# Optimization experiments

Measured on AMD Instinct MI355X. Metric: run time of the kernel, lower is better.

## Reference

```python
import jax, jax.numpy as jnp
import numpy as np

B, H, E = 1024, 2048, 1024

def _xavier(key, shape):
    # torch xavier_normal_ on [1, out, in]: std = sqrt(2/(fan_in+fan_out)) over last two dims
    fan_out, fan_in = shape[-2], shape[-1]
    std = (2.0 / (fan_in + fan_out)) ** 0.5
    return jax.random.normal(key, shape, jnp.float32) * std

def setup_inputs() -> dict:
    key = jax.random.key(0)
    ks = jax.random.split(key, 17)
    inp = {
        'x': jax.random.normal(ks[0], (B, E, 1), jnp.float32),
        'c': jax.random.normal(ks[1], (B, H, 1), jnp.float32),
        'h': jax.random.normal(ks[2], (B, H, 1), jnp.float32),
        'W_xi': _xavier(ks[3], (1, H, E)), 'W_hi': _xavier(ks[4], (1, H, H)), 'B_i': _xavier(ks[5], (1, H, 1)),
        'W_xg': _xavier(ks[6], (1, H, E)), 'W_hg': _xavier(ks[7], (1, H, H)), 'B_g': _xavier(ks[8], (1, H, 1)),
        'W_xf': _xavier(ks[9], (1, H, E)), 'W_hf': _xavier(ks[10], (1, H, H)), 'B_f': _xavier(ks[11], (1, H, 1)),
        'W_xo': _xavier(ks[12], (1, H, E)), 'W_ho': _xavier(ks[13], (1, H, H)), 'B_o': _xavier(ks[14], (1, H, 1)),
        'W_hy': _xavier(ks[15], (1, E, H)), 'B_y': _xavier(ks[16], (1, E, 1)),
    }
    return inp

def reference(x, c, h, W_xi, W_hi, B_i, W_xg, W_hg, B_g, W_xf, W_hf, B_f, W_xo, W_ho, B_o, W_hy, B_y):
    # jnp.matmul broadcasts the leading batch dim: [1,H,E] @ [B,E,1] -> [B,H,1]
    i = jax.nn.sigmoid(jnp.matmul(W_xi, x) + jnp.matmul(W_hi, h) + B_i)
    g = jnp.tanh(jnp.matmul(W_xg, x) + jnp.matmul(W_hg, h) + B_g)
    f = jax.nn.sigmoid(jnp.matmul(W_xf, x) + jnp.matmul(W_hf, h) + B_f)
    c_new = f * c + i * g
    o = jax.nn.sigmoid(jnp.matmul(W_xo, x) + jnp.matmul(W_ho, h) + B_o)
    h_new = o * c_new  # NOTE: source uses o*c (no tanh), faithful to original
    y = jnp.tanh(jnp.matmul(W_hy, h_new) + B_y)
    return (y, c_new, h_new)
```

## Files before the change

### kernel.cpp

```cpp
#include <hip/hip_runtime.h>

#define B_SZ 1024
#define H_SZ 2048
#define E_SZ 1024

typedef float  f32x4 __attribute__((ext_vector_type(4)));
typedef short  s16x8 __attribute__((ext_vector_type(8)));

__device__ __forceinline__ unsigned short f2bf(float f) {
    unsigned u = __float_as_uint(f);
    u = u + 0x7fffu + ((u >> 16) & 1u);
    return (unsigned short)(u >> 16);
}
__device__ __forceinline__ float bf2f(unsigned short s) {
    return __uint_as_float(((unsigned)s) << 16);
}
__device__ __forceinline__ float sigm(float v) {
    return 1.0f / (1.0f + __expf(-v));
}
__device__ __forceinline__ unsigned cvtpk(float lo, float hi) {
    unsigned r;
    asm("v_cvt_pk_bf16_f32 %0, %1, %2" : "=v"(r) : "v"(lo), "v"(hi));
    return r;
}

__device__ __forceinline__ void gll(const unsigned short* g, unsigned short* l) {
    __builtin_amdgcn_global_load_lds(
        (const __attribute__((address_space(1))) unsigned int*)g,
        (__attribute__((address_space(3))) unsigned int*)l, 16, 0, 0);
}

struct CastArgs {
    const float*    src[2];
    unsigned short* dst[2];
    int             n[2];
};

__global__ __launch_bounds__(256) void cast_kernel(CastArgs a) {
    const int arr = blockIdx.y;
    const int n = a.n[arr];
    const float* __restrict__ s = a.src[arr];
    unsigned short* __restrict__ d = a.dst[arr];
    const int stride = gridDim.x * 256 * 4;
    for (int i = (blockIdx.x * 256 + threadIdx.x) * 4; i < n; i += stride) {
        float4 v = *(const float4*)(s + i);
        ushort4 o;
        o.x = f2bf(v.x); o.y = f2bf(v.y); o.z = f2bf(v.z); o.w = f2bf(v.w);
        *(ushort4*)(d + i) = o;
    }
}

__device__ __forceinline__ void gemm_bk128(
    const unsigned short* __restrict__ A,
    const float* __restrict__ W,
    int ld, int kLen, int m0, int n0,
    unsigned short* lA, unsigned short* lB,
    f32x4 acc[4][4], int t)
{
    const int lane = t & 63;
    const int w    = t >> 6;
    const int wr   = (w >> 1) << 6;
    const int wc   = (w & 1) << 6;
    const int lr   = lane & 15;
    const int q4   = lane >> 4;

    const int srow = t >> 4;
    const int sblk = ((t & 15) ^ srow) << 3;
    const unsigned short* gA = A + (size_t)(m0 + srow) * ld + sblk;
    const float*          gW = W + (size_t)(n0 + srow) * ld + sblk;
    const size_t st16 = (size_t)16 * ld;

    f32x4 f0[8], f1[8];
#pragma unroll
    for (int p = 0; p < 8; ++p) {
        const float* s = gW + p * st16;
        f0[p] = *(const f32x4*)(s);
        f1[p] = *(const f32x4*)(s + 4);
    }

    for (int k0 = 0; k0 < kLen; k0 += 128) {
#pragma unroll
        for (int p = 0; p < 8; ++p) {
            uint4 pk;
            pk.x = cvtpk(f0[p].x, f0[p].y);
            pk.y = cvtpk(f0[p].z, f0[p].w);
            pk.z = cvtpk(f1[p].x, f1[p].y);
            pk.w = cvtpk(f1[p].z, f1[p].w);
            *(uint4*)(lB + (t + 256 * p) * 8) = pk;
        }
#pragma unroll
        for (int p = 0; p < 8; ++p)
            gll(gA + k0 + p * st16, lA + (t + 256 * p) * 8);
        __syncthreads();

        if (k0 + 128 < kLen) {
#pragma unroll
            for (int p = 0; p < 8; ++p) {
                const float* s = gW + (k0 + 128) + p * st16;
                f0[p] = *(const f32x4*)(s);
                f1[p] = *(const f32x4*)(s + 4);
            }
        }

#pragma unroll
        for (int ks = 0; ks < 4; ++ks) {
            s16x8 af[4], bfr[4];
#pragma unroll
            for (int i = 0; i < 4; ++i) {
                const int ra = wr + i * 16 + lr;
                af[i] = *(const s16x8*)(lA + ra * 128 +
                         ((((ks << 2) + q4) ^ (ra & 15)) << 3));
            }
#pragma unroll
            for (int j = 0; j < 4; ++j) {
                const int rb = wc + j * 16 + lr;
                bfr[j] = *(const s16x8*)(lB + rb * 128 +
                          ((((ks << 2) + q4) ^ (rb & 15)) << 3));
            }
#pragma unroll
            for (int i = 0; i < 4; ++i)
#pragma unroll
                for (int j = 0; j < 4; ++j)
                    acc[i][j] = __builtin_amdgcn_mfma_f32_16x16x32_bf16(
                        af[i], bfr[j], acc[i][j], 0, 0, 0);
        }
        __syncthreads();
    }
}

struct GatesArgs {
    const unsigned short *Xb, *Hb;
    const float *Wx[4], *Wh[4], *bias[4];
    unsigned short *Z;
};

__global__ __launch_bounds__(256, 2) void gates_kernel(GatesArgs a) {
    __shared__ unsigned short lA[128 * 128];
    __shared__ unsigned short lB[128 * 128];
    const int t   = threadIdx.x;
    const int b   = blockIdx.x;
    const int xcd = b & 7;
    const int i_  = b >> 3;
    const int nt  = xcd * 8 + (i_ >> 3);
    const int m0  = (i_ & 7) * 128;
    const int q   = nt >> 4;
    const int n0  = (nt & 15) * 128;

    f32x4 acc[4][4] = {};
    gemm_bk128(a.Xb, a.Wx[q], E_SZ, E_SZ, m0, n0, lA, lB, acc, t);
    gemm_bk128(a.Hb, a.Wh[q], H_SZ, H_SZ, m0, n0, lA, lB, acc, t);

    const float* bias = a.bias[q];
    const int lane = t & 63, w = t >> 6;
    const int wr = (w >> 1) << 6, wc = (w & 1) << 6;
    const int lr = lane & 15, rq = (lane >> 4) << 2;
    unsigned short* Zq = a.Z + (size_t)q * B_SZ * H_SZ;
#pragma unroll
    for (int i = 0; i < 4; ++i) {
#pragma unroll
        for (int j = 0; j < 4; ++j) {
            const int n = n0 + wc + j * 16 + lr;
            const float bv = bias[n];
#pragma unroll
            for (int r = 0; r < 4; ++r) {
                const int m = m0 + wr + i * 16 + rq + r;
                const float v = acc[i][j][r] + bv;
                const float act = (q == 1) ? tanhf(v) : sigm(v);
                Zq[(size_t)m * H_SZ + n] = f2bf(act);
            }
        }
    }
}

__global__ __launch_bounds__(256) void cell_kernel(
    const unsigned short* __restrict__ Z, const float* __restrict__ c,
    float* __restrict__ c_out, float* __restrict__ h_out,
    unsigned short* __restrict__ HnB)
{
    const size_t BH = (size_t)B_SZ * H_SZ;
    const int idx = (blockIdx.x * 256 + threadIdx.x) * 4;
    ushort4 iu = *(const ushort4*)(Z + idx);
    ushort4 gu = *(const ushort4*)(Z + BH + idx);
    ushort4 fu = *(const ushort4*)(Z + 2 * BH + idx);
    ushort4 ou = *(const ushort4*)(Z + 3 * BH + idx);
    float4 cv = *(const float4*)(c + idx);

    float cn[4], hn[4];
    cn[0] = bf2f(fu.x) * cv.x + bf2f(iu.x) * bf2f(gu.x);
    cn[1] = bf2f(fu.y) * cv.y + bf2f(iu.y) * bf2f(gu.y);
    cn[2] = bf2f(fu.z) * cv.z + bf2f(iu.z) * bf2f(gu.z);
    cn[3] = bf2f(fu.w) * cv.w + bf2f(iu.w) * bf2f(gu.w);
    hn[0] = bf2f(ou.x) * cn[0];
    hn[1] = bf2f(ou.y) * cn[1];
    hn[2] = bf2f(ou.z) * cn[2];
    hn[3] = bf2f(ou.w) * cn[3];

    *(float4*)(c_out + idx) = make_float4(cn[0], cn[1], cn[2], cn[3]);
    *(float4*)(h_out + idx) = make_float4(hn[0], hn[1], hn[2], hn[3]);
    ushort4 hb;
    hb.x = f2bf(hn[0]); hb.y = f2bf(hn[1]); hb.z = f2bf(hn[2]); hb.w = f2bf(hn[3]);
    *(ushort4*)(HnB + idx) = hb;
}

__global__ __launch_bounds__(256, 2) void y_split_kernel(
    const unsigned short* __restrict__ Hn,
    const float* __restrict__ Wy,
    float* __restrict__ part)
{
    __shared__ unsigned short lA[128 * 128];
    __shared__ unsigned short lB[128 * 128];
    const int t   = threadIdx.x;
    const int b   = blockIdx.x;
    const int xcd = b & 7;
    const int i_  = b >> 3;
    const int ns  = xcd * 4 + (i_ >> 3);
    const int m0  = (i_ & 7) * 128;
    const int n0  = (ns >> 2) * 128;
    const int s   = ns & 3;

    f32x4 acc[4][4] = {};
    gemm_bk128(Hn + s * 512, Wy + s * 512, H_SZ, 512, m0, n0, lA, lB, acc, t);

    const int lane = t & 63, w = t >> 6;
    const int wr = (w >> 1) << 6, wc = (w & 1) << 6;
    const int lr = lane & 15, rq = (lane >> 4) << 2;
    float* P = part + (size_t)s * B_SZ * E_SZ;
#pragma unroll
    for (int i = 0; i < 4; ++i) {
#pragma unroll
        for (int j = 0; j < 4; ++j) {
            const int n = n0 + wc + j * 16 + lr;
#pragma unroll
            for (int r = 0; r < 4; ++r) {
                const int m = m0 + wr + i * 16 + rq + r;
                P[(size_t)m * E_SZ + n] = acc[i][j][r];
            }
        }
    }
}

__global__ __launch_bounds__(256) void y_reduce_kernel(
    const float* __restrict__ part, const float* __restrict__ by,
    float* __restrict__ yout)
{
    const size_t BE = (size_t)B_SZ * E_SZ;
    const int idx = (blockIdx.x * 256 + threadIdx.x) * 4;
    float4 a = *(const float4*)(part + idx);
    float4 b2 = *(const float4*)(part + BE + idx);
    float4 c2 = *(const float4*)(part + 2 * BE + idx);
    float4 d2 = *(const float4*)(part + 3 * BE + idx);
    const int col = idx & (E_SZ - 1);
    float4 bv = *(const float4*)(by + col);
    float4 o;
    o.x = tanhf(a.x + b2.x + c2.x + d2.x + bv.x);
    o.y = tanhf(a.y + b2.y + c2.y + d2.y + bv.y);
    o.z = tanhf(a.z + b2.z + c2.z + d2.z + bv.z);
    o.w = tanhf(a.w + b2.w + c2.w + d2.w + bv.w);
    *(float4*)(yout + idx) = o;
}

extern "C" void kernel_launch(void* const* d_in, const int* in_sizes, int n_in,
                              void* d_out, int out_size, void* d_ws, size_t ws_size,
                              hipStream_t stream) {
    const float* x   = (const float*)d_in[0];
    const float* c   = (const float*)d_in[1];
    const float* h   = (const float*)d_in[2];
    const float* Wxi = (const float*)d_in[3];
    const float* Whi = (const float*)d_in[4];
    const float* Bi  = (const float*)d_in[5];
    const float* Wxg = (const float*)d_in[6];
    const float* Whg = (const float*)d_in[7];
    const float* Bg  = (const float*)d_in[8];
    const float* Wxf = (const float*)d_in[9];
    const float* Whf = (const float*)d_in[10];
    const float* Bf  = (const float*)d_in[11];
    const float* Wxo = (const float*)d_in[12];
    const float* Who = (const float*)d_in[13];
    const float* Bo  = (const float*)d_in[14];
    const float* Why = (const float*)d_in[15];
    const float* By  = (const float*)d_in[16];

    const size_t BE = (size_t)B_SZ * E_SZ, BH = (size_t)B_SZ * H_SZ;

    unsigned short* ws  = (unsigned short*)d_ws;
    unsigned short* Xb  = ws;
    unsigned short* Hb  = Xb + BE;
    unsigned short* Z   = Hb + BH;
    unsigned short* HnB = Z + 4 * BH;

    CastArgs ca;
    ca.src[0] = x; ca.dst[0] = Xb; ca.n[0] = (int)BE;
    ca.src[1] = h; ca.dst[1] = Hb; ca.n[1] = (int)BH;
    hipLaunchKernelGGL(cast_kernel, dim3(512, 2), dim3(256), 0, stream, ca);

    GatesArgs ga;
    ga.Xb = Xb; ga.Hb = Hb;
    ga.Wx[0] = Wxi; ga.Wx[1] = Wxg; ga.Wx[2] = Wxf; ga.Wx[3] = Wxo;
    ga.Wh[0] = Whi; ga.Wh[1] = Whg; ga.Wh[2] = Whf; ga.Wh[3] = Who;
    ga.bias[0] = Bi; ga.bias[1] = Bg; ga.bias[2] = Bf; ga.bias[3] = Bo;
    ga.Z = Z;
    hipLaunchKernelGGL(gates_kernel, dim3(512), dim3(256), 0, stream, ga);

    float* y_out = (float*)d_out;
    float* c_out = y_out + BE;
    float* h_out = c_out + BH;
    hipLaunchKernelGGL(cell_kernel, dim3((unsigned)(BH / 1024)), dim3(256), 0, stream,
                       Z, c, c_out, h_out, HnB);

    float* ypart = (float*)Z;
    hipLaunchKernelGGL(y_split_kernel, dim3(256), dim3(256), 0, stream,
                       HnB, Why, ypart);
    hipLaunchKernelGGL(y_reduce_kernel, dim3((unsigned)(BE / 1024)), dim3(256), 0, stream,
                       ypart, By, y_out);
}
```

Before: 274.5 us.

## Fuse gate GEMMs with LSTM cell update and pre-cast weights to bf16

The four gate GEMMs now share one block: each block computes 32 columns of every gate, so the cell update (c_new, h_new, and h_new in bf16) runs in the epilogue from shared memory. This removes the intermediate Z gate buffer and the separate cell kernel. The gate and hidden weights are now cast to bf16 in the cast kernel every call, which adds an extra pass over roughly 24M floats. The K-tile shrinks from 128 to 64.

```diff
diff --git a/kernel.cpp b/kernel.cpp
--- a/kernel.cpp
+++ b/kernel.cpp
@@ -31,9 +31,9 @@
 }
 
 struct CastArgs {
-    const float*    src[2];
-    unsigned short* dst[2];
-    int             n[2];
+    const float*    src[10];
+    unsigned short* dst[10];
+    int             n[10];
 };
 
 __global__ __launch_bounds__(256) void cast_kernel(CastArgs a) {
@@ -47,6 +47,154 @@
         ushort4 o;
         o.x = f2bf(v.x); o.y = f2bf(v.y); o.z = f2bf(v.z); o.w = f2bf(v.w);
         *(ushort4*)(d + i) = o;
+    }
+}
+
+__device__ __forceinline__ void gemm_gates4(
+    const unsigned short* __restrict__ A,
+    const unsigned short* __restrict__ W0,
+    const unsigned short* __restrict__ W1,
+    const unsigned short* __restrict__ W2,
+    const unsigned short* __restrict__ W3,
+    int ld, int kLen, int m0, int n0h,
+    unsigned short* lA, unsigned short* lB,
+    f32x4 acc[4][4], int t)
+{
+    const int lane = t & 63;
+    const int w    = t >> 6;
+    const int wr   = (w >> 1) << 6;
+    const int wc   = (w & 1) << 6;
+    const int lr   = lane & 15;
+    const int q4   = lane >> 4;
+
+    const int srow = t >> 3;
+    const int scol = ((t & 7) ^ (srow & 7)) << 3;
+    const unsigned short* gA = A + (size_t)(m0 + srow) * ld + scol;
+    const size_t st32 = (size_t)32 * ld;
+    const size_t boff = (size_t)(n0h + srow) * ld + scol;
+    const unsigned short* gB0 = W0 + boff;
+    const unsigned short* gB1 = W1 + boff;
+    const unsigned short* gB2 = W2 + boff;
+    const unsigned short* gB3 = W3 + boff;
+
+    const int cb0 = ((q4    ) ^ (lr & 7)) << 3;
+    const int cb1 = ((4 + q4) ^ (lr & 7)) << 3;
+
+    for (int k0 = 0; k0 < kLen; k0 += 64) {
+#pragma unroll
+        for (int p = 0; p < 4; ++p)
+            gll(gA + k0 + p * st32, lA + (t + 256 * p) * 8);
+        gll(gB0 + k0, lB + t * 8);
+        gll(gB1 + k0, lB + (t + 256) * 8);
+        gll(gB2 + k0, lB + (t + 512) * 8);
+        gll(gB3 + k0, lB + (t + 768) * 8);
+        __syncthreads();
+
+#pragma unroll
+        for (int ks = 0; ks < 2; ++ks) {
+            const int cb = ks ? cb1 : cb0;
+            s16x8 af[4], bfr[4];
+#pragma unroll
+            for (int i = 0; i < 4; ++i)
+                af[i] = *(const s16x8*)(lA + (wr + i * 16 + lr) * 64 + cb);
+#pragma unroll
+            for (int j = 0; j < 4; ++j)
+                bfr[j] = *(const s16x8*)(lB + (wc + j * 16 + lr) * 64 + cb);
+#pragma unroll
+            for (int i = 0; i < 4; ++i)
+#pragma unroll
+                for (int j = 0; j < 4; ++j)
+                    acc[i][j] = __builtin_amdgcn_mfma_f32_16x16x32_bf16(
+                        af[i], bfr[j], acc[i][j], 0, 0, 0);
+        }
+        __syncthreads();
+    }
+}
+
+struct GatesCellArgs {
+    const unsigned short *Xb, *Hb, *Wxb, *Whb;
+    const float *bias[4];
+    const float *cin;
+    float *c_out, *h_out;
+    unsigned short *HnB;
+};
+
+__global__ __launch_bounds__(256, 2) void gates_cell_kernel(GatesCellArgs a) {
+    __shared__ unsigned short smem[16384];
+    unsigned short* lA = smem;
+    unsigned short* lB = smem + 8192;
+
+    const int t   = threadIdx.x;
+    const int b   = blockIdx.x;
+    const int xcd = b & 7;
+    const int i_  = b >> 3;
+    const int nt  = xcd * 8 + (i_ >> 3);
+    const int m0  = (i_ & 7) * 128;
+    const int n0h = nt * 32;
+
+    const size_t HE = (size_t)H_SZ * E_SZ, HH = (size_t)H_SZ * H_SZ;
+
+    f32x4 acc[4][4] = {};
+    gemm_gates4(a.Xb, a.Wxb, a.Wxb + HE, a.Wxb + 2 * HE, a.Wxb + 3 * HE,
+                E_SZ, E_SZ, m0, n0h, lA, lB, acc, t);
+    gemm_gates4(a.Hb, a.Whb, a.Whb + HH, a.Whb + 2 * HH, a.Whb + 3 * HH,
+                H_SZ, H_SZ, m0, n0h, lA, lB, acc, t);
+
+    const int lane = t & 63, w = t >> 6;
+    const int wr = (w >> 1) << 6, wc = (w & 1) << 6;
+    const int lr = lane & 15, rq = (lane >> 4) << 2;
+#pragma unroll
+    for (int j = 0; j < 4; ++j) {
+        const int col = wc + j * 16 + lr;
+        const int q   = col >> 5;
+        const float bv = a.bias[q][n0h + (col & 31)];
+#pragma unroll
+        for (int i = 0; i < 4; ++i) {
+#pragma unroll
+            for (int r = 0; r < 4; ++r) {
+                const int row = wr + i * 16 + rq + r;
+                const float v = acc[i][j][r] + bv;
+                const float act = (q == 1) ? tanhf(v) : sigm(v);
+                smem[row * 128 + col] = f2bf(act);
+            }
+        }
+    }
+    __syncthreads();
+
+    {
+        const int row = t >> 1;
+        const int hc  = (t & 1) * 16;
+        const unsigned short* ex = smem + row * 128;
+        s16x8 i0 = *(const s16x8*)(ex + hc);
+        s16x8 i1 = *(const s16x8*)(ex + hc + 8);
+        s16x8 g0 = *(const s16x8*)(ex + 32 + hc);
+        s16x8 g1 = *(const s16x8*)(ex + 32 + hc + 8);
+        s16x8 fg0 = *(const s16x8*)(ex + 64 + hc);
+        s16x8 fg1 = *(const s16x8*)(ex + 64 + hc + 8);
+        s16x8 o0 = *(const s16x8*)(ex + 96 + hc);
+        s16x8 o1 = *(const s16x8*)(ex + 96 + hc + 8);
+
+        const size_t gidx = (size_t)(m0 + row) * H_SZ + n0h + hc;
+        float cn[16], hn[16];
+#pragma unroll
+        for (int k = 0; k < 16; ++k) {
+            const float iv = bf2f((unsigned short)((k < 8 ? i0[k] : i1[k - 8])));
+            const float gv = bf2f((unsigned short)((k < 8 ? g0[k] : g1[k - 8])));
+            const float fv = bf2f((unsigned short)((k < 8 ? fg0[k] : fg1[k - 8])));
+            const float ov = bf2f((unsigned short)((k < 8 ? o0[k] : o1[k - 8])));
+            const float cv = a.cin[gidx + k];
+            cn[k] = fv * cv + iv * gv;
+            hn[k] = ov * cn[k];
+        }
+#pragma unroll
+        for (int k = 0; k < 16; k += 4) {
+            *(float4*)(a.c_out + gidx + k) = make_float4(cn[k], cn[k+1], cn[k+2], cn[k+3]);
+            *(float4*)(a.h_out + gidx + k) = make_float4(hn[k], hn[k+1], hn[k+2], hn[k+3]);
+            ushort4 hb;
+            hb.x = f2bf(hn[k]);     hb.y = f2bf(hn[k+1]);
+            hb.z = f2bf(hn[k+2]);   hb.w = f2bf(hn[k+3]);
+            *(ushort4*)(a.HnB + gidx + k) = hb;
+        }
     }
 }
 
@@ -126,80 +274,6 @@
         }
         __syncthreads();
     }
-}
-
-struct GatesArgs {
-    const unsigned short *Xb, *Hb;
-    const float *Wx[4], *Wh[4], *bias[4];
-    unsigned short *Z;
-};
-
-__global__ __launch_bounds__(256, 2) void gates_kernel(GatesArgs a) {
-    __shared__ unsigned short lA[128 * 128];
-    __shared__ unsigned short lB[128 * 128];
-    const int t   = threadIdx.x;
-    const int b   = blockIdx.x;
-    const int xcd = b & 7;
-    const int i_  = b >> 3;
-    const int nt  = xcd * 8 + (i_ >> 3);
-    const int m0  = (i_ & 7) * 128;
-    const int q   = nt >> 4;
-    const int n0  = (nt & 15) * 128;
-
-    f32x4 acc[4][4] = {};
-    gemm_bk128(a.Xb, a.Wx[q], E_SZ, E_SZ, m0, n0, lA, lB, acc, t);
-    gemm_bk128(a.Hb, a.Wh[q], H_SZ, H_SZ, m0, n0, lA, lB, acc, t);
-
-    const float* bias = a.bias[q];
-    const int lane = t & 63, w = t >> 6;
-    const int wr = (w >> 1) << 6, wc = (w & 1) << 6;
-    const int lr = lane & 15, rq = (lane >> 4) << 2;
-    unsigned short* Zq = a.Z + (size_t)q * B_SZ * H_SZ;
-#pragma unroll
-    for (int i = 0; i < 4; ++i) {
-#pragma unroll
-        for (int j = 0; j < 4; ++j) {
-            const int n = n0 + wc + j * 16 + lr;
-            const float bv = bias[n];
-#pragma unroll
-            for (int r = 0; r < 4; ++r) {
-                const int m = m0 + wr + i * 16 + rq + r;
-                const float v = acc[i][j][r] + bv;
-                const float act = (q == 1) ? tanhf(v) : sigm(v);
-                Zq[(size_t)m * H_SZ + n] = f2bf(act);
-            }
-        }
-    }
-}
-
-__global__ __launch_bounds__(256) void cell_kernel(
-    const unsigned short* __restrict__ Z, const float* __restrict__ c,
-    float* __restrict__ c_out, float* __restrict__ h_out,
-    unsigned short* __restrict__ HnB)
-{
-    const size_t BH = (size_t)B_SZ * H_SZ;
-    const int idx = (blockIdx.x * 256 + threadIdx.x) * 4;
-    ushort4 iu = *(const ushort4*)(Z + idx);
-    ushort4 gu = *(const ushort4*)(Z + BH + idx);
-    ushort4 fu = *(const ushort4*)(Z + 2 * BH + idx);
-    ushort4 ou = *(const ushort4*)(Z + 3 * BH + idx);
-    float4 cv = *(const float4*)(c + idx);
-
-    float cn[4], hn[4];
-    cn[0] = bf2f(fu.x) * cv.x + bf2f(iu.x) * bf2f(gu.x);
-    cn[1] = bf2f(fu.y) * cv.y + bf2f(iu.y) * bf2f(gu.y);
-    cn[2] = bf2f(fu.z) * cv.z + bf2f(iu.z) * bf2f(gu.z);
-    cn[3] = bf2f(fu.w) * cv.w + bf2f(iu.w) * bf2f(gu.w);
-    hn[0] = bf2f(ou.x) * cn[0];
-    hn[1] = bf2f(ou.y) * cn[1];
-    hn[2] = bf2f(ou.z) * cn[2];
-    hn[3] = bf2f(ou.w) * cn[3];
-
-    *(float4*)(c_out + idx) = make_float4(cn[0], cn[1], cn[2], cn[3]);
-    *(float4*)(h_out + idx) = make_float4(hn[0], hn[1], hn[2], hn[3]);
-    ushort4 hb;
-    hb.x = f2bf(hn[0]); hb.y = f2bf(hn[1]); hb.z = f2bf(hn[2]); hb.w = f2bf(hn[3]);
-    *(ushort4*)(HnB + idx) = hb;
 }
 
 __global__ __launch_bounds__(256, 2) void y_split_kernel(
@@ -281,33 +355,39 @@
     const float* By  = (const float*)d_in[16];
 
     const size_t BE = (size_t)B_SZ * E_SZ, BH = (size_t)B_SZ * H_SZ;
+    const size_t HE = (size_t)H_SZ * E_SZ, HH = (size_t)H_SZ * H_SZ;
 
     unsigned short* ws  = (unsigned short*)d_ws;
     unsigned short* Xb  = ws;
     unsigned short* Hb  = Xb + BE;
-    unsigned short* Z   = Hb + BH;
-    unsigned short* HnB = Z + 4 * BH;
+    unsigned short* Wxb = Hb + BH;
+    unsigned short* Whb = Wxb + 4 * HE;
+    unsigned short* HnB = Whb + 4 * HH;
+    float*          ypart = (float*)(HnB + BH);
 
     CastArgs ca;
-    ca.src[0] = x; ca.dst[0] = Xb; ca.n[0] = (int)BE;
-    ca.src[1] = h; ca.dst[1] = Hb; ca.n[1] = (int)BH;
-    hipLaunchKernelGGL(cast_kernel, dim3(512, 2), dim3(256), 0, stream, ca);
-
-    GatesArgs ga;
-    ga.Xb = Xb; ga.Hb = Hb;
-    ga.Wx[0] = Wxi; ga.Wx[1] = Wxg; ga.Wx[2] = Wxf; ga.Wx[3] = Wxo;
-    ga.Wh[0] = Whi; ga.Wh[1] = Whg; ga.Wh[2] = Whf; ga.Wh[3] = Who;
-    ga.bias[0] = Bi; ga.bias[1] = Bg; ga.bias[2] = Bf; ga.bias[3] = Bo;
-    ga.Z = Z;
-    hipLaunchKernelGGL(gates_kernel, dim3(512), dim3(256), 0, stream, ga);
+    ca.src[0] = x;   ca.dst[0] = Xb;          ca.n[0] = (int)BE;
+    ca.src[1] = h;   ca.dst[1] = Hb;          ca.n[1] = (int)BH;
+    ca.src[2] = Wxi; ca.dst[2] = Wxb;         ca.n[2] = (int)HE;
+    ca.src[3] = Wxg; ca.dst[3] = Wxb + HE;    ca.n[3] = (int)HE;
+    ca.src[4] = Wxf; ca.dst[4] = Wxb + 2*HE;  ca.n[4] = (int)HE;
+    ca.src[5] = Wxo; ca.dst[5] = Wxb + 3*HE;  ca.n[5] = (int)HE;
+    ca.src[6] = Whi; ca.dst[6] = Whb;         ca.n[6] = (int)HH;
+    ca.src[7] = Whg; ca.dst[7] = Whb + HH;    ca.n[7] = (int)HH;
+    ca.src[8] = Whf; ca.dst[8] = Whb + 2*HH;  ca.n[8] = (int)HH;
+    ca.src[9] = Who; ca.dst[9] = Whb + 3*HH;  ca.n[9] = (int)HH;
+    hipLaunchKernelGGL(cast_kernel, dim3(512, 10), dim3(256), 0, stream, ca);
 
     float* y_out = (float*)d_out;
     float* c_out = y_out + BE;
     float* h_out = c_out + BH;
-    hipLaunchKernelGGL(cell_kernel, dim3((unsigned)(BH / 1024)), dim3(256), 0, stream,
-                       Z, c, c_out, h_out, HnB);
-
-    float* ypart = (float*)Z;
+
+    GatesCellArgs ga;
+    ga.Xb = Xb; ga.Hb = Hb; ga.Wxb = Wxb; ga.Whb = Whb;
+    ga.bias[0] = Bi; ga.bias[1] = Bg; ga.bias[2] = Bf; ga.bias[3] = Bo;
+    ga.cin = c; ga.c_out = c_out; ga.h_out = h_out; ga.HnB = HnB;
+    hipLaunchKernelGGL(gates_cell_kernel, dim3(512), dim3(256), 0, stream, ga);
+
     hipLaunchKernelGGL(y_split_kernel, dim3(256), dim3(256), 0, stream,
                        HnB, Why, ypart);
     hipLaunchKernelGGL(y_reduce_kernel, dim3((unsigned)(BE / 1024)), dim3(256), 0, stream,
```

After: 262.4 us. 4.4% less time.
